# Performance work log

Hardware: AMD Instinct MI355X
Metric: run time of the kernel (lower is better)

The kernel has to match this reference:

```python
import jax, jax.numpy as jnp
import numpy as np

B, T, D = 8, 2048, 512
DK = 128
FENETRES = (24, 168, 720)
EPS = 1e-5


def setup_inputs() -> dict:
    key = jax.random.key(0)
    ks = jax.random.split(key, 8)
    s = 0.02
    return {
        "x": jax.random.normal(ks[0], (B, T, D), dtype=jnp.float32),
        "Wq": jax.random.normal(ks[1], (D, DK), dtype=jnp.float32) * s,
        "bq": jnp.zeros((DK,), dtype=jnp.float32),
        "Wk": jax.random.normal(ks[2], (D, DK), dtype=jnp.float32) * s,
        "bk": jnp.zeros((DK,), dtype=jnp.float32),
        "Wo": jax.random.normal(ks[3], (D, D), dtype=jnp.float32) * s,
        "bo": jnp.zeros((D,), dtype=jnp.float32),
        "gamma": jnp.ones((D,), dtype=jnp.float32),
        "beta": jnp.zeros((D,), dtype=jnp.float32),
    }


def reference(x, Wq, bq, Wk, bk, Wo, bo, gamma, beta):
    # projections (dropout is identity in eval mode)
    q = x @ Wq + bq                      # [B,T,DK]
    k = x @ Wk + bk                      # [B,T,DK]
    dk = q.shape[-1]
    # scores are identical across window scales; compute once
    scores = jnp.einsum('btd,bsd->bts', q, k) / jnp.sqrt(jnp.float32(dk))
    t = jnp.arange(x.shape[1])
    dist = jnp.abs(t[:, None] - t[None, :])  # [T,T]
    acc = jnp.zeros_like(x)
    for w in FENETRES:
        band = dist <= (w // 2)              # row i attends to [i-w//2, i+w//2]
        s = jnp.where(band[None, :, :], scores, jnp.float32(-1e9))
        attn = jax.nn.softmax(s, axis=-1)    # [B,T,T]
        acc = acc + jnp.einsum('bts,bsd->btd', attn, x)
    acc = acc / jnp.float32(len(FENETRES))
    out = acc @ Wo + bo
    res = x + out
    # LayerNorm over last dim, eps=1e-5
    mu = jnp.mean(res, axis=-1, keepdims=True)
    var = jnp.mean(jnp.square(res - mu), axis=-1, keepdims=True)
    return (res - mu) * jax.lax.rsqrt(var + EPS) * gamma + beta
```

## Files before the change

### kernel.cpp

```cpp
#include <hip/hip_runtime.h>

typedef unsigned short u16;
typedef __attribute__((ext_vector_type(4))) unsigned short u16x4;
typedef __attribute__((ext_vector_type(8))) unsigned short u16x8;
typedef __attribute__((ext_vector_type(8))) short bf16x8;
typedef __attribute__((ext_vector_type(4))) float f32x4;

constexpr int Bn = 8, Tn = 2048, Dn = 512, DKn = 128;
constexpr int QB = 64;
constexpr int WJ = 832;
constexpr int NCH = 13;
constexpr int WQB = 16;
constexpr int WST = 776;

__device__ inline u16 f2bf(float f) {
  unsigned u = __float_as_uint(f);
  return (u16)((u + 0x7FFFu + ((u >> 16) & 1u)) >> 16);
}
__device__ inline float bf2f(u16 h) {
  return __uint_as_float(((unsigned)h) << 16);
}
__device__ inline void gload16(const void* g, void* l) {
  __builtin_amdgcn_global_load_lds(
      (const __attribute__((address_space(1))) unsigned int*)g,
      (__attribute__((address_space(3))) unsigned int*)l, 16, 0, 0);
}
__device__ inline f32x4 mfma16(bf16x8 a, bf16x8 b, f32x4 c) {
  return __builtin_amdgcn_mfma_f32_16x16x32_bf16(a, b, c, 0, 0, 0);
}

__global__ __launch_bounds__(256) void xpose_kernel(
    const float* __restrict__ x, u16* __restrict__ xT, u16* __restrict__ xbf) {
  __shared__ u16 tile[64][72];
  const int blk = blockIdx.x;
  const int b = blk >> 8;
  const int rem = blk & 255;
  const int t0 = (rem >> 3) * 64, d0 = (rem & 7) * 64;
  const int tid = threadIdx.x;

#pragma unroll
  for (int it = 0; it < 4; ++it) {
    int r = (tid >> 4) + it * 16;
    int c = (tid & 15) * 4;
    float4 v = *(const float4*)&x[(size_t)(b * Tn + t0 + r) * Dn + d0 + c];
    u16 b0 = f2bf(v.x), b1 = f2bf(v.y), b2 = f2bf(v.z), b3 = f2bf(v.w);
    tile[c + 0][r] = b0;
    tile[c + 1][r] = b1;
    tile[c + 2][r] = b2;
    tile[c + 3][r] = b3;
    u16x4 pv; pv[0] = b0; pv[1] = b1; pv[2] = b2; pv[3] = b3;
    *(u16x4*)&xbf[(size_t)(b * Tn + t0 + r) * Dn + d0 + c] = pv;
  }
  __syncthreads();
  const int dr = tid >> 2, ts = (tid & 3) * 16;
  u16x8 v0 = *(const u16x8*)&tile[dr][ts];
  u16x8 v1 = *(const u16x8*)&tile[dr][ts + 8];
  u16* dst = xT + (size_t)(b * Dn + d0 + dr) * Tn + t0 + ts;
  *(u16x8*)dst = v0;
  *(u16x8*)(dst + 8) = v1;
}

__global__ __launch_bounds__(256) void wprep_kernel(
    const float* __restrict__ Wq, const float* __restrict__ Wk,
    const float* __restrict__ Wo,
    u16* __restrict__ WqkT, u16* __restrict__ WoTf) {
  __shared__ u16 tile[64][72];
  const int tid = threadIdx.x;
  const int blk = blockIdx.x;
  const float* src;
  int srcC, r0, c0, rowOff;
  if (blk < 32) {
    src = (blk < 16) ? Wq : Wk;
    rowOff = (blk < 16) ? 0 : 128;
    int t = blk & 15;
    r0 = (t >> 1) * 64; c0 = (t & 1) * 64;
    srcC = 128;
  } else {
    int t = blk - 32;
    src = Wo; rowOff = 0;
    r0 = (t >> 3) * 64; c0 = (t & 7) * 64;
    srcC = 512;
  }
#pragma unroll
  for (int it = 0; it < 4; ++it) {
    int r = (tid >> 4) + it * 16;
    int c = (tid & 15) * 4;
    float4 v = *(const float4*)&src[(size_t)(r0 + r) * srcC + c0 + c];
    tile[c + 0][r] = f2bf(v.x);
    tile[c + 1][r] = f2bf(v.y);
    tile[c + 2][r] = f2bf(v.z);
    tile[c + 3][r] = f2bf(v.w);
  }
  __syncthreads();
  const int dr = tid >> 2, ts = (tid & 3) * 16;
  u16x8 v0 = *(const u16x8*)&tile[dr][ts];
  u16x8 v1 = *(const u16x8*)&tile[dr][ts + 8];
  if (blk < 32) {
    u16* dp = WqkT + (size_t)(rowOff + c0 + dr) * 512 + r0 + ts;
    *(u16x8*)dp = v0;
    *(u16x8*)(dp + 8) = v1;
  } else {
    int n = c0 + dr;
    int d0 = r0 + ts, d1 = d0 + 8;
    size_t a0 = (size_t)(((n >> 4) * 16 + (d0 >> 5)) * 64 +
                         ((((d0 >> 3) & 3) << 4) | (n & 15))) * 8;
    size_t a1 = (size_t)(((n >> 4) * 16 + (d1 >> 5)) * 64 +
                         ((((d1 >> 3) & 3) << 4) | (n & 15))) * 8;
    *(u16x8*)&WoTf[a0] = v0;
    *(u16x8*)&WoTf[a1] = v1;
  }
}

__global__ __launch_bounds__(512) void qk_mfma_kernel(
    const u16* __restrict__ xbf, const u16* __restrict__ WqkT,
    const float* __restrict__ bq, const float* __restrict__ bk,
    u16* __restrict__ qbf, u16* __restrict__ kbf) {
  __shared__ u16 as_[2][64 * 64];
  __shared__ u16 bs_[2][256 * 64];
  const int tid = threadIdx.x, w = tid >> 6, l = tid & 63;
  const int r0 = blockIdx.x * 64;
  const int wr = w >> 2, wc = w & 3;

  f32x4 acc[2][4];
#pragma unroll
  for (int mm = 0; mm < 2; ++mm)
#pragma unroll
    for (int n = 0; n < 4; ++n) acc[mm][n] = (f32x4){0.f, 0.f, 0.f, 0.f};

  auto stageA = [&](int c, int buf) {
    int row = 8 * w + (l >> 3);
    int ss = (l & 7) ^ (row & 7);
    gload16(xbf + ((size_t)(r0 + row) * Dn + c * 64 + ss * 8),
            (char*)&as_[buf][0] + w * 1024);
  };
  auto stageB = [&](int c, int buf) {
#pragma unroll
    for (int ii = 0; ii < 4; ++ii) {
      int i = 4 * w + ii;
      int n = i * 8 + (l >> 3);
      int ss = (l & 7) ^ (n & 7);
      gload16(WqkT + ((size_t)n * Dn + c * 64 + ss * 8),
              (char*)&bs_[buf][0] + i * 1024);
    }
  };
  stageA(0, 0); stageB(0, 0);
  __syncthreads();
  for (int c = 0; c < 8; ++c) {
    if (c + 1 < 8) { stageA(c + 1, (c + 1) & 1); stageB(c + 1, (c + 1) & 1); }
    const u16* ab = &as_[c & 1][0];
    const u16* bb = &bs_[c & 1][0];
#pragma unroll
    for (int kk = 0; kk < 2; ++kk) {
      int rA0 = wr * 32 + (l & 15);
      int sA = ((l >> 4) + 4 * kk) ^ (rA0 & 7);
      bf16x8 a0 = *(const bf16x8*)(ab + rA0 * 64 + sA * 8);
      bf16x8 a1 = *(const bf16x8*)(ab + (rA0 + 16) * 64 + sA * 8);
#pragma unroll
      for (int n = 0; n < 4; ++n) {
        int rB = wc * 64 + n * 16 + (l & 15);
        int sB = ((l >> 4) + 4 * kk) ^ (rB & 7);
        bf16x8 bv = *(const bf16x8*)(bb + rB * 64 + sB * 8);
        acc[0][n] = mfma16(a0, bv, acc[0][n]);
        acc[1][n] = mfma16(a1, bv, acc[1][n]);
      }
    }
    __syncthreads();
  }
#pragma unroll
  for (int n = 0; n < 4; ++n) {
    int col = wc * 64 + n * 16 + (l & 15);
    float bias = (col < 128) ? bq[col] : bk[col - 128];
    u16* outp = (col < 128) ? (qbf + col) : (kbf + col - 128);
#pragma unroll
    for (int mm = 0; mm < 2; ++mm)
#pragma unroll
      for (int i = 0; i < 4; ++i) {
        int row = r0 + wr * 32 + mm * 16 + 4 * (l >> 4) + i;
        outp[(size_t)row * DKn] = f2bf(acc[mm][n][i] + bias);
      }
  }
}

__global__ __launch_bounds__(256) void weights_kernel(
    const u16* __restrict__ qbf, const u16* __restrict__ kbf,
    u16* __restrict__ Wg) {
  __shared__ u16 S[WQB * WST];
  __shared__ float spart[4][WQB][3];
  const int tid = threadIdx.x, w = tid >> 6, l = tid & 63;
  const int blk = (blockIdx.x & 7) * 128 + (blockIdx.x >> 3);
  const int b = blk >> 7;
  const int tt = blk & 127;
  const int t0 = tt * WQB;
  const int jbase = t0 - 360;
  const float scale = 0.08838834764831845f;

  bf16x8 a[4];
  {
    int row = t0 + (l & 15);
    const u16* qp = qbf + (size_t)(b * Tn + row) * DKn + (l >> 4) * 8;
#pragma unroll
    for (int kk = 0; kk < 4; ++kk) a[kk] = *(const bf16x8*)(qp + kk * 32);
  }

  float s0[4], s1[4], s2[4];
#pragma unroll
  for (int i = 0; i < 4; ++i) { s0[i] = 0.f; s1[i] = 0.f; s2[i] = 0.f; }
  const int rbase = 4 * (l >> 4);

  for (int c = 0; c < 12; ++c) {
    int jj = c * 64 + w * 16 + (l & 15);
    int j = jbase + jj;
    int jc = j < 0 ? 0 : (j > Tn - 1 ? Tn - 1 : j);
    const u16* kp = kbf + (size_t)(b * Tn + jc) * DKn + (l >> 4) * 8;
    f32x4 acc = {0.f, 0.f, 0.f, 0.f};
#pragma unroll
    for (int kk = 0; kk < 4; ++kk)
      acc = mfma16(a[kk], *(const bf16x8*)(kp + kk * 32), acc);
    bool valid = (j >= 0) && (j < Tn);
#pragma unroll
    for (int i = 0; i < 4; ++i) {
      int r = rbase + i;
      int dist = jj - r - 360; dist = dist < 0 ? -dist : dist;
      float e = __expf(acc[i] * scale);
      e = (valid && dist <= 360) ? e : 0.f;
      S[r * WST + jj] = f2bf(e);
      bool in0 = dist <= 12, in1 = dist <= 84;
      s0[i] += in0 ? e : 0.f;
      s1[i] += (in1 && !in0) ? e : 0.f;
      s2[i] += in1 ? 0.f : e;
    }
  }

#pragma unroll
  for (int o = 1; o < 16; o <<= 1)
#pragma unroll
    for (int i = 0; i < 4; ++i) {
      s0[i] += __shfl_xor(s0[i], o);
      s1[i] += __shfl_xor(s1[i], o);
      s2[i] += __shfl_xor(s2[i], o);
    }
  if ((l & 15) == 0) {
#pragma unroll
    for (int i = 0; i < 4; ++i) {
      spart[w][rbase + i][0] = s0[i];
      spart[w][rbase + i][1] = s1[i];
      spart[w][rbase + i][2] = s2[i];
    }
  }
  __syncthreads();

  const int off = (tt & 3) * 16;
  const int pvblk = b * 32 + (tt >> 2);
#pragma unroll
  for (int rr = 0; rr < 4; ++rr) {
    int r = 4 * w + rr;
    float L0 = spart[0][r][0] + spart[1][r][0] + spart[2][r][0] + spart[3][r][0];
    float L1 = L0 + spart[0][r][1] + spart[1][r][1] + spart[2][r][1] + spart[3][r][1];
    float L2 = L1 + spart[0][r][2] + spart[1][r][2] + spart[2][r][2] + spart[3][r][2];
    float F2 = (1.f / 3.f) / L2;
    float F1 = (1.f / 3.f) / L1 + F2;
    float F0 = (1.f / 3.f) / L0 + F1;
    const int center = r + 360;
    u16* wrow = Wg + ((size_t)pvblk * QB + off + r) * WJ;
#pragma unroll
    for (int t = 0; t < 6; ++t) {
      int jjw = 2 * l + 128 * t;
      if (jjw < 736) {
        unsigned pv2 = *(const unsigned*)&S[r * WST + jjw];
        float e0 = bf2f((u16)(pv2 & 0xffff));
        float e1 = bf2f((u16)(pv2 >> 16));
        int d0 = jjw - center; d0 = d0 < 0 ? -d0 : d0;
        int d1 = jjw + 1 - center; d1 = d1 < 0 ? -d1 : d1;
        float c0 = e0 * (d0 <= 12 ? F0 : (d0 <= 84 ? F1 : F2));
        float c1 = e1 * (d1 <= 12 ? F0 : (d1 <= 84 ? F1 : F2));
        unsigned o2 = (unsigned)f2bf(c0) | ((unsigned)f2bf(c1) << 16);
        *(unsigned*)&wrow[off + jjw] = o2;
      }
    }
    if (l < 48) {
      int jjp = (l < (off >> 1)) ? 2 * l : 736 + 2 * l;
      *(unsigned*)&wrow[jjp] = 0u;
    }
  }
}

__global__ __launch_bounds__(512) void pv_kernel(
    const u16* __restrict__ Wg, const u16* __restrict__ xT,
    u16* __restrict__ accbf) {
  __shared__ u16 xs[2][256 * 64];
  __shared__ u16 ws[2][QB * 64];
  const int tid = threadIdx.x;
  const int w = tid >> 6, l = tid & 63;
  const int work = (blockIdx.x & 7) * 64 + (blockIdx.x >> 3);
  const int b = work >> 6;
  const int rem = work & 63;
  const int tt = rem >> 1;
  const int dh = rem & 1;
  const int t064 = tt * QB;
  const int jbase = t064 - 360;
  const int pvblk = b * 32 + tt;
  const int wr = w >> 2, wc = w & 3;

  f32x4 acc[2][4];
#pragma unroll
  for (int mm = 0; mm < 2; ++mm)
#pragma unroll
    for (int n = 0; n < 4; ++n) acc[mm][n] = (f32x4){0.f,0.f,0.f,0.f};

  auto stage = [&](int c, int buf) {
#pragma unroll
    for (int ii = 0; ii < 4; ++ii) {
      int i = 4 * w + ii;
      int d = i * 8 + (l >> 3);
      int ss = (l & 7) ^ (d & 7);
      int g = jbase + c * 64 + ss * 8;
      g = g < 0 ? 0 : (g > Tn - 8 ? Tn - 8 : g);
      gload16(xT + ((size_t)(b * Dn + dh * 256 + d) * Tn + g),
              (char*)&xs[buf][0] + i * 1024);
    }
    int row = 8 * w + (l >> 3);
    int ss = (l & 7) ^ (row & 7);
    gload16(Wg + ((size_t)(pvblk * QB + row)) * WJ + c * 64 + ss * 8,
            (char*)&ws[buf][0] + w * 1024);
  };

  stage(0, 0);
  __syncthreads();
  for (int c = 0; c < NCH; ++c) {
    if (c + 1 < NCH) stage(c + 1, (c + 1) & 1);
    const u16* xb = &xs[c & 1][0];
    const u16* wb = &ws[c & 1][0];
#pragma unroll
    for (int kk = 0; kk < 2; ++kk) {
      int rA0 = wr * 32 + (l & 15);
      int sA = ((l >> 4) + 4 * kk) ^ (rA0 & 7);
      bf16x8 a0 = *(const bf16x8*)(wb + rA0 * 64 + sA * 8);
      bf16x8 a1 = *(const bf16x8*)(wb + (rA0 + 16) * 64 + sA * 8);
#pragma unroll
      for (int n = 0; n < 4; ++n) {
        int rB = wc * 64 + n * 16 + (l & 15);
        int sB = ((l >> 4) + 4 * kk) ^ (rB & 7);
        bf16x8 bv = *(const bf16x8*)(xb + rB * 64 + sB * 8);
        acc[0][n] = mfma16(a0, bv, acc[0][n]);
        acc[1][n] = mfma16(a1, bv, acc[1][n]);
      }
    }
    __syncthreads();
  }
#pragma unroll
  for (int mm = 0; mm < 2; ++mm)
#pragma unroll
    for (int n = 0; n < 4; ++n)
#pragma unroll
      for (int i = 0; i < 4; ++i) {
        int row = wr * 32 + mm * 16 + 4 * (l >> 4) + i;
        int col = dh * 256 + wc * 64 + n * 16 + (l & 15);
        accbf[(size_t)(b * Tn + t064 + row) * Dn + col] = f2bf(acc[mm][n][i]);
      }
}

__global__ __launch_bounds__(512, 4) void out_ln_mfma_kernel(
    const u16* __restrict__ accbf, const float* __restrict__ x,
    const u16* __restrict__ WoTf, const float* __restrict__ bo,
    const float* __restrict__ gamma, const float* __restrict__ beta,
    float* __restrict__ out) {
  __shared__ float red[32][8][2];
  const int tid = threadIdx.x, w = tid >> 6, l = tid & 63;
  const int r0 = blockIdx.x * 32;

  f32x4 acc[4][2];
#pragma unroll
  for (int m = 0; m < 4; ++m)
#pragma unroll
    for (int nh = 0; nh < 2; ++nh) acc[m][nh] = (f32x4){0.f,0.f,0.f,0.f};

  const u16* aptr = WoTf + (size_t)(w * 4) * 16 * 512 + l * 8;
  const u16* bptr = accbf + (size_t)(r0 + (l & 15)) * Dn + (l >> 4) * 8;

#pragma unroll 4
  for (int c = 0; c < 16; ++c) {
    bf16x8 bfr[2];
#pragma unroll
    for (int nh = 0; nh < 2; ++nh)
      bfr[nh] = *(const bf16x8*)(bptr + (size_t)nh * 16 * Dn + c * 32);
#pragma unroll
    for (int m = 0; m < 4; ++m) {
      bf16x8 afr = *(const bf16x8*)(aptr + (size_t)(m * 16 + c) * 512);
      acc[m][0] = mfma16(afr, bfr[0], acc[m][0]);
      acc[m][1] = mfma16(afr, bfr[1], acc[m][1]);
    }
  }

  float s[2] = {0.f, 0.f}, s2[2] = {0.f, 0.f};
#pragma unroll
  for (int nh = 0; nh < 2; ++nh) {
    int trow_g = r0 + nh * 16 + (l & 15);
#pragma unroll
    for (int m = 0; m < 4; ++m) {
      int outc = w * 64 + m * 16 + (l >> 4) * 4;
      float4 xq  = *(const float4*)&x[(size_t)trow_g * Dn + outc];
      float4 bo4 = *(const float4*)&bo[outc];
      acc[m][nh][0] += bo4.x + xq.x;
      acc[m][nh][1] += bo4.y + xq.y;
      acc[m][nh][2] += bo4.z + xq.z;
      acc[m][nh][3] += bo4.w + xq.w;
#pragma unroll
      for (int i = 0; i < 4; ++i) {
        float v = acc[m][nh][i];
        s[nh] += v; s2[nh] += v * v;
      }
    }
  }
#pragma unroll
  for (int nh = 0; nh < 2; ++nh) {
    s[nh]  += __shfl_xor(s[nh], 16);  s[nh]  += __shfl_xor(s[nh], 32);
    s2[nh] += __shfl_xor(s2[nh], 16); s2[nh] += __shfl_xor(s2[nh], 32);
  }
  if (l < 16) {
#pragma unroll
    for (int nh = 0; nh < 2; ++nh) {
      red[nh * 16 + l][w][0] = s[nh];
      red[nh * 16 + l][w][1] = s2[nh];
    }
  }
  __syncthreads();
#pragma unroll
  for (int nh = 0; nh < 2; ++nh) {
    int trow = nh * 16 + (l & 15);
    float ts = 0.f, ts2 = 0.f;
#pragma unroll
    for (int ww = 0; ww < 8; ++ww) {
      ts  += red[trow][ww][0];
      ts2 += red[trow][ww][1];
    }
    float mean = ts * (1.f / 512.f);
    float var  = ts2 * (1.f / 512.f) - mean * mean;
    float inv  = rsqrtf(var + 1e-5f);
    size_t grow = (size_t)(r0 + trow) * Dn;
#pragma unroll
    for (int m = 0; m < 4; ++m) {
      int outc = w * 64 + m * 16 + (l >> 4) * 4;
      float4 g4  = *(const float4*)&gamma[outc];
      float4 be4 = *(const float4*)&beta[outc];
      float4 o4;
      o4.x = (acc[m][nh][0] - mean) * inv * g4.x + be4.x;
      o4.y = (acc[m][nh][1] - mean) * inv * g4.y + be4.y;
      o4.z = (acc[m][nh][2] - mean) * inv * g4.z + be4.z;
      o4.w = (acc[m][nh][3] - mean) * inv * g4.w + be4.w;
      *(float4*)&out[grow + outc] = o4;
    }
  }
}

extern "C" void kernel_launch(void* const* d_in, const int* in_sizes, int n_in,
                              void* d_out, int out_size, void* d_ws, size_t ws_size,
                              hipStream_t stream) {
  const float* x     = (const float*)d_in[0];
  const float* Wq    = (const float*)d_in[1];
  const float* bq    = (const float*)d_in[2];
  const float* Wk    = (const float*)d_in[3];
  const float* bk    = (const float*)d_in[4];
  const float* Wo    = (const float*)d_in[5];
  const float* bo    = (const float*)d_in[6];
  const float* gamma = (const float*)d_in[7];
  const float* beta  = (const float*)d_in[8];
  float* out = (float*)d_out;

  u16* qbf   = (u16*)d_ws;
  u16* kbf   = qbf   + (size_t)Bn * Tn * DKn;
  u16* xT    = kbf   + (size_t)Bn * Tn * DKn;
  u16* xbf   = xT    + (size_t)Bn * Dn * Tn;
  u16* Wg    = xbf   + (size_t)Bn * Tn * Dn;
  u16* accbf = Wg    + (size_t)Bn * 32 * QB * WJ;
  u16* WqkT  = accbf + (size_t)Bn * Tn * Dn;
  u16* WoTf  = WqkT  + (size_t)256 * 512;

  xpose_kernel<<<Bn * 256, 256, 0, stream>>>(x, xT, xbf);
  wprep_kernel<<<96, 256, 0, stream>>>(Wq, Wk, Wo, WqkT, WoTf);
  qk_mfma_kernel<<<Bn * Tn / 64, 512, 0, stream>>>(xbf, WqkT, bq, bk, qbf, kbf);
  weights_kernel<<<Bn * 128, 256, 0, stream>>>(qbf, kbf, Wg);
  pv_kernel<<<Bn * 64, 512, 0, stream>>>(Wg, xT, accbf);
  out_ln_mfma_kernel<<<Bn * Tn / 32, 512, 0, stream>>>(accbf, x, WoTf, bo, gamma, beta, out);
}
```

Baseline: 120.7 us.

## Rewrite QK projection to read pre-fragmented weights directly, drop LDS staging

The Wq/Wk weights are now stored in the same MFMA-fragment-ordered layout already used for Wo, so the QK projection kernel can load A fragments straight from global memory. That kernel no longer uses double-buffered LDS staging or barriers. It uses 32-row blocks with 256 threads, reads x fragments directly from global, and writes vectorised 4-wide bf16 outputs with bias. The intent is to remove LDS traffic and synchronisation overhead and to improve occupancy. The cost is more global and L2 reads, because the weights are no longer shared through LDS.

```diff
diff --git a/kernel.cpp b/kernel.cpp
--- a/kernel.cpp
+++ b/kernel.cpp
@@ -63,7 +63,7 @@
 __global__ __launch_bounds__(256) void wprep_kernel(
     const float* __restrict__ Wq, const float* __restrict__ Wk,
     const float* __restrict__ Wo,
-    u16* __restrict__ WqkT, u16* __restrict__ WoTf) {
+    u16* __restrict__ WqkTf, u16* __restrict__ WoTf) {
   __shared__ u16 tile[64][72];
   const int tid = threadIdx.x;
   const int blk = blockIdx.x;
@@ -95,89 +95,64 @@
   const int dr = tid >> 2, ts = (tid & 3) * 16;
   u16x8 v0 = *(const u16x8*)&tile[dr][ts];
   u16x8 v1 = *(const u16x8*)&tile[dr][ts + 8];
-  if (blk < 32) {
-    u16* dp = WqkT + (size_t)(rowOff + c0 + dr) * 512 + r0 + ts;
-    *(u16x8*)dp = v0;
-    *(u16x8*)(dp + 8) = v1;
-  } else {
-    int n = c0 + dr;
-    int d0 = r0 + ts, d1 = d0 + 8;
-    size_t a0 = (size_t)(((n >> 4) * 16 + (d0 >> 5)) * 64 +
-                         ((((d0 >> 3) & 3) << 4) | (n & 15))) * 8;
-    size_t a1 = (size_t)(((n >> 4) * 16 + (d1 >> 5)) * 64 +
-                         ((((d1 >> 3) & 3) << 4) | (n & 15))) * 8;
-    *(u16x8*)&WoTf[a0] = v0;
-    *(u16x8*)&WoTf[a1] = v1;
-  }
-}
-
-__global__ __launch_bounds__(512) void qk_mfma_kernel(
-    const u16* __restrict__ xbf, const u16* __restrict__ WqkT,
+  int n = rowOff + c0 + dr;
+  int d0 = r0 + ts, d1 = d0 + 8;
+  size_t a0 = (size_t)(((n >> 4) * 16 + (d0 >> 5)) * 64 +
+                       ((((d0 >> 3) & 3) << 4) | (n & 15))) * 8;
+  size_t a1 = (size_t)(((n >> 4) * 16 + (d1 >> 5)) * 64 +
+                       ((((d1 >> 3) & 3) << 4) | (n & 15))) * 8;
+  u16* dst = (blk < 32) ? WqkTf : WoTf;
+  *(u16x8*)&dst[a0] = v0;
+  *(u16x8*)&dst[a1] = v1;
+}
+
+__global__ __launch_bounds__(256, 4) void qk_mfma_kernel(
+    const u16* __restrict__ xbf, const u16* __restrict__ WqkTf,
     const float* __restrict__ bq, const float* __restrict__ bk,
     u16* __restrict__ qbf, u16* __restrict__ kbf) {
-  __shared__ u16 as_[2][64 * 64];
-  __shared__ u16 bs_[2][256 * 64];
   const int tid = threadIdx.x, w = tid >> 6, l = tid & 63;
-  const int r0 = blockIdx.x * 64;
-  const int wr = w >> 2, wc = w & 3;
-
-  f32x4 acc[2][4];
-#pragma unroll
-  for (int mm = 0; mm < 2; ++mm)
-#pragma unroll
-    for (int n = 0; n < 4; ++n) acc[mm][n] = (f32x4){0.f, 0.f, 0.f, 0.f};
-
-  auto stageA = [&](int c, int buf) {
-    int row = 8 * w + (l >> 3);
-    int ss = (l & 7) ^ (row & 7);
-    gload16(xbf + ((size_t)(r0 + row) * Dn + c * 64 + ss * 8),
-            (char*)&as_[buf][0] + w * 1024);
-  };
-  auto stageB = [&](int c, int buf) {
-#pragma unroll
-    for (int ii = 0; ii < 4; ++ii) {
-      int i = 4 * w + ii;
-      int n = i * 8 + (l >> 3);
-      int ss = (l & 7) ^ (n & 7);
-      gload16(WqkT + ((size_t)n * Dn + c * 64 + ss * 8),
-              (char*)&bs_[buf][0] + i * 1024);
-    }
-  };
-  stageA(0, 0); stageB(0, 0);
-  __syncthreads();
-  for (int c = 0; c < 8; ++c) {
-    if (c + 1 < 8) { stageA(c + 1, (c + 1) & 1); stageB(c + 1, (c + 1) & 1); }
-    const u16* ab = &as_[c & 1][0];
-    const u16* bb = &bs_[c & 1][0];
-#pragma unroll
-    for (int kk = 0; kk < 2; ++kk) {
-      int rA0 = wr * 32 + (l & 15);
-      int sA = ((l >> 4) + 4 * kk) ^ (rA0 & 7);
-      bf16x8 a0 = *(const bf16x8*)(ab + rA0 * 64 + sA * 8);
-      bf16x8 a1 = *(const bf16x8*)(ab + (rA0 + 16) * 64 + sA * 8);
-#pragma unroll
-      for (int n = 0; n < 4; ++n) {
-        int rB = wc * 64 + n * 16 + (l & 15);
-        int sB = ((l >> 4) + 4 * kk) ^ (rB & 7);
-        bf16x8 bv = *(const bf16x8*)(bb + rB * 64 + sB * 8);
-        acc[0][n] = mfma16(a0, bv, acc[0][n]);
-        acc[1][n] = mfma16(a1, bv, acc[1][n]);
-      }
-    }
-    __syncthreads();
-  }
-#pragma unroll
-  for (int n = 0; n < 4; ++n) {
-    int col = wc * 64 + n * 16 + (l & 15);
-    float bias = (col < 128) ? bq[col] : bk[col - 128];
-    u16* outp = (col < 128) ? (qbf + col) : (kbf + col - 128);
-#pragma unroll
-    for (int mm = 0; mm < 2; ++mm)
-#pragma unroll
-      for (int i = 0; i < 4; ++i) {
-        int row = r0 + wr * 32 + mm * 16 + 4 * (l >> 4) + i;
-        outp[(size_t)row * DKn] = f2bf(acc[mm][n][i] + bias);
-      }
+  const int r0 = blockIdx.x * 32;
+
+  f32x4 acc[4][2];
+#pragma unroll
+  for (int m = 0; m < 4; ++m)
+#pragma unroll
+    for (int nh = 0; nh < 2; ++nh) acc[m][nh] = (f32x4){0.f,0.f,0.f,0.f};
+
+  const u16* aptr = WqkTf + (size_t)(w * 4) * 16 * 512 + l * 8;
+  const u16* bptr = xbf + (size_t)(r0 + (l & 15)) * Dn + (l >> 4) * 8;
+
+#pragma unroll 4
+  for (int c = 0; c < 16; ++c) {
+    bf16x8 bfr[2];
+#pragma unroll
+    for (int nh = 0; nh < 2; ++nh)
+      bfr[nh] = *(const bf16x8*)(bptr + (size_t)nh * 16 * Dn + c * 32);
+#pragma unroll
+    for (int m = 0; m < 4; ++m) {
+      bf16x8 afr = *(const bf16x8*)(aptr + (size_t)(m * 16 + c) * 512);
+      acc[m][0] = mfma16(afr, bfr[0], acc[m][0]);
+      acc[m][1] = mfma16(afr, bfr[1], acc[m][1]);
+    }
+  }
+
+  u16* outp = (w < 2) ? qbf : kbf;
+  const float* bias = (w < 2) ? bq : bk;
+#pragma unroll
+  for (int m = 0; m < 4; ++m) {
+    int outc = w * 64 + m * 16 + (l >> 4) * 4;
+    int lc = outc & 127;
+    float4 b4 = *(const float4*)&bias[lc];
+#pragma unroll
+    for (int nh = 0; nh < 2; ++nh) {
+      int row = r0 + nh * 16 + (l & 15);
+      u16x4 o;
+      o[0] = f2bf(acc[m][nh][0] + b4.x);
+      o[1] = f2bf(acc[m][nh][1] + b4.y);
+      o[2] = f2bf(acc[m][nh][2] + b4.z);
+      o[3] = f2bf(acc[m][nh][3] + b4.w);
+      *(u16x4*)&outp[(size_t)row * DKn + lc] = o;
+    }
   }
 }
 
@@ -472,12 +447,12 @@
   u16* xbf   = xT    + (size_t)Bn * Dn * Tn;
   u16* Wg    = xbf   + (size_t)Bn * Tn * Dn;
   u16* accbf = Wg    + (size_t)Bn * 32 * QB * WJ;
-  u16* WqkT  = accbf + (size_t)Bn * Tn * Dn;
-  u16* WoTf  = WqkT  + (size_t)256 * 512;
+  u16* WqkTf = accbf + (size_t)Bn * Tn * Dn;
+  u16* WoTf  = WqkTf + (size_t)256 * 512;
 
   xpose_kernel<<<Bn * 256, 256, 0, stream>>>(x, xT, xbf);
-  wprep_kernel<<<96, 256, 0, stream>>>(Wq, Wk, Wo, WqkT, WoTf);
-  qk_mfma_kernel<<<Bn * Tn / 64, 512, 0, stream>>>(xbf, WqkT, bq, bk, qbf, kbf);
+  wprep_kernel<<<96, 256, 0, stream>>>(Wq, Wk, Wo, WqkTf, WoTf);
+  qk_mfma_kernel<<<Bn * Tn / 32, 256, 0, stream>>>(xbf, WqkTf, bq, bk, qbf, kbf);
   weights_kernel<<<Bn * 128, 256, 0, stream>>>(qbf, kbf, Wg);
   pv_kernel<<<Bn * 64, 512, 0, stream>>>(Wg, xT, accbf);
   out_ln_mfma_kernel<<<Bn * Tn / 32, 512, 0, stream>>>(accbf, x, WoTf, bo, gamma, beta, out);
```

Result: slower. 125.3 us (+3.8%).
